# Kernel tuning notes

Hardware: AMD Instinct MI355X
Metric: run time of the kernel (lower is better)

The kernel has to match this reference:

```python
import jax, jax.numpy as jnp
import numpy as np

# Multi-scale feature pyramid spatial shapes (h, w) per level; static for jit.
SPATIAL_SHAPES = np.array([[64, 176], [32, 88], [16, 44], [8, 22]], dtype=np.int32)


def setup_inputs() -> dict:
    key = jax.random.key(0)
    k1, k2 = jax.random.split(key)
    bs, num_heads, head_dim = 6, 8, 32          # 6 cams, embed_dim 256
    num_queries, num_levels, num_points = 40000, 4, 4  # 200x200 BEV grid, 4 Z anchors
    num_keys = int((SPATIAL_SHAPES[:, 0] * SPATIAL_SHAPES[:, 1]).sum())  # 14960
    value = jax.random.normal(k1, (bs, num_keys, num_heads, head_dim), jnp.float32)
    # normalized sampling locations in [0,1] (x, y)
    sampling_locations = jax.random.uniform(
        k2, (bs, num_queries, num_heads, num_levels, num_points, 2), jnp.float32)
    value_spatial_shapes = jnp.asarray(SPATIAL_SHAPES)
    return {"value": value,
            "value_spatial_shapes": value_spatial_shapes,
            "sampling_locations": sampling_locations}


def _msda(value, sampling_locations):
    """Multi-scale deformable attention, nearest sampling, zero padding,
    align_corners=False (matches F.grid_sample defaults used in the source).
    value: (bs, num_keys, H, D); sampling_locations: (bs, nq, H, L, P, 2).
    Returns (bs, nq, H*D)."""
    bs, _, H, D = value.shape
    _, nq, _, num_levels, P, _ = sampling_locations.shape
    grids = 2.0 * sampling_locations - 1.0  # -> [-1, 1]
    out = jnp.zeros((bs, H, nq, D), value.dtype)
    offset = 0
    for lvl in range(num_levels):
        h, w = int(SPATIAL_SHAPES[lvl, 0]), int(SPATIAL_SHAPES[lvl, 1])
        # (bs, h*w, H, D) -> (bs, H, h*w, D)
        v = jnp.transpose(value[:, offset:offset + h * w], (0, 2, 1, 3))
        g = grids[:, :, :, lvl]                      # (bs, nq, H, P, 2)
        # unnormalize (align_corners=False): pix = ((g+1)*size - 1)/2
        x = (g[..., 0] + 1.0) * w * 0.5 - 0.5
        y = (g[..., 1] + 1.0) * h * 0.5 - 0.5
        ix = jnp.rint(x).astype(jnp.int32)
        iy = jnp.rint(y).astype(jnp.int32)
        valid = (ix >= 0) & (ix < w) & (iy >= 0) & (iy < h)
        idx = jnp.clip(iy, 0, h - 1) * w + jnp.clip(ix, 0, w - 1)  # (bs, nq, H, P)
        idx = jnp.transpose(idx, (0, 2, 1, 3)).reshape(bs, H, nq * P)
        sampled = jnp.take_along_axis(v, idx[..., None], axis=2)  # (bs, H, nq*P, D)
        mask = jnp.transpose(valid, (0, 2, 1, 3)).reshape(bs, H, nq * P, 1)
        sampled = jnp.where(mask, sampled, 0.0).reshape(bs, H, nq, P, D)
        out = out + sampled.sum(axis=3)  # sum over points; accumulating over levels
        offset += h * w
    # (bs, H, nq, D) -> (bs, nq, H*D)
    return jnp.transpose(out, (0, 2, 1, 3)).reshape(bs, nq, H * D)


def reference(value, value_spatial_shapes, sampling_locations):
    # value_spatial_shapes matches the static SPATIAL_SHAPES constant used for
    # level splitting (shapes must be static under jit).
    return _msda(value, sampling_locations)
```

## Files before the change

### kernel.cpp

```cpp
#include <hip/hip_runtime.h>


#define BS 6
#define NQ 40000
#define NH 8
#define HD 32
#define NK 14960

typedef float f32x4 __attribute__((ext_vector_type(4)));

__global__ __launch_bounds__(256, 4)
void msda_kernel(const float* __restrict__ value,
                 const float* __restrict__ loc,
                 float* __restrict__ out) {
    const int tid = blockIdx.x * 256 + threadIdx.x;
    const int dg  = tid & 7;
    const int g   = tid >> 3;
    const int h   = g & 7;
    const int bq  = g >> 3;
    const int b   = bq / NQ;

    const int lane = threadIdx.x & 63;
    const int ll   = lane & 7;

    const f32x4 myL = *(const f32x4*)(loc + (size_t)g * 32 + ll * 4);

    const int l   = ll >> 1;
    const int W   = 176 >> l;
    const int Hh  = 64  >> l;
    const int off = (45056 - (45056 >> (2 * l))) / 3;
    const float wf = (float)W, hf = (float)Hh;

    int koff[2];
    #pragma unroll
    for (int j = 0; j < 2; ++j) {
        const float px = j ? myL.z : myL.x;
        const float py = j ? myL.w : myL.y;
        const float gx = 2.0f * px - 1.0f;
        const float gy = 2.0f * py - 1.0f;
        const float x  = ((gx + 1.0f) * wf) * 0.5f - 0.5f;
        const float y  = ((gy + 1.0f) * hf) * 0.5f - 0.5f;
        const float fx = rintf(x);
        const float fy = rintf(y);
        const int ix = (int)fx;
        const int iy = (int)fy;
        const bool valid = (ix >= 0) & (ix < W) & (iy >= 0) & (iy < Hh);
        const int cx = min(max(ix, 0), W - 1);
        const int cy = min(max(iy, 0), Hh - 1);
        const int key = off + cy * W + cx;
        koff[j] = (key << 10) | (valid ? 1 : 0);
    }

    const int srcbase = lane & 56;
    int ko[16];
    #pragma unroll
    for (int s = 0; s < 16; ++s)
        ko[s] = __shfl(koff[s & 1], srcbase + (s >> 1), 64);

    const unsigned base_off = (unsigned)b * (NK * NH * HD * 4u)
                            + (unsigned)h * (HD * 4u)
                            + (unsigned)dg * 16u;

    f32x4 v[16];
    #pragma unroll
    for (int s = 0; s < 16; ++s) {
        const unsigned a = base_off + ((unsigned)ko[s] & 0xFFFFFFFEu);
        v[s] = *(const f32x4*)((const char*)value + a);
    }
    asm volatile(""
        : "+v"(v[0]),  "+v"(v[1]),  "+v"(v[2]),  "+v"(v[3]),
          "+v"(v[4]),  "+v"(v[5]),  "+v"(v[6]),  "+v"(v[7]),
          "+v"(v[8]),  "+v"(v[9]),  "+v"(v[10]), "+v"(v[11]),
          "+v"(v[12]), "+v"(v[13]), "+v"(v[14]), "+v"(v[15]));

    f32x4 acc = {0.f, 0.f, 0.f, 0.f};
    #pragma unroll
    for (int s = 0; s < 16; ++s) {
        const float w = (float)(ko[s] & 1);
        acc.x = fmaf(v[s].x, w, acc.x);
        acc.y = fmaf(v[s].y, w, acc.y);
        acc.z = fmaf(v[s].z, w, acc.z);
        acc.w = fmaf(v[s].w, w, acc.w);
    }

    *(f32x4*)(out + (size_t)g * HD + dg * 4) = acc;
}

extern "C" void kernel_launch(void* const* d_in, const int* in_sizes, int n_in,
                              void* d_out, int out_size, void* d_ws, size_t ws_size,
                              hipStream_t stream) {
    const float* value = (const float*)d_in[0];
    const float* loc   = (const float*)d_in[2];
    float* out = (float*)d_out;

    msda_kernel<<<60000, 256, 0, stream>>>(value, loc, out);
}
```

Baseline: 620.6 us.

## Process two query-head groups per thread with nontemporal loc loads and output stores

Each thread now handles two (batch,query,head) groups 32 apart, issuing 32 gathered value loads in flight instead of 16. The grid is halved and the launch bound is relaxed to allow more registers. Validity bits are packed into a bitmask, and the streaming location reads and output writes use nontemporal hints to keep value data resident in cache. This buys more memory-level parallelism per thread at the cost of higher register pressure and lower occupancy.

```diff
diff --git a/kernel.cpp b/kernel.cpp
--- a/kernel.cpp
+++ b/kernel.cpp
@@ -9,21 +9,24 @@
 
 typedef float f32x4 __attribute__((ext_vector_type(4)));
 
-__global__ __launch_bounds__(256, 4)
+__global__ __launch_bounds__(256, 2)
 void msda_kernel(const float* __restrict__ value,
                  const float* __restrict__ loc,
                  float* __restrict__ out) {
-    const int tid = blockIdx.x * 256 + threadIdx.x;
-    const int dg  = tid & 7;
-    const int g   = tid >> 3;
-    const int h   = g & 7;
-    const int bq  = g >> 3;
-    const int b   = bq / NQ;
+    const int t  = threadIdx.x;
+    const int ll = t & 7;
+    const int gi = t >> 3;
+    const int g0 = blockIdx.x * 64 + gi;
+    const int g1 = g0 + 32;
+    const int h  = g0 & 7;
+    const int b  = g0 / 320000;
 
-    const int lane = threadIdx.x & 63;
-    const int ll   = lane & 7;
+    const int lane = t & 63;
 
-    const f32x4 myL = *(const f32x4*)(loc + (size_t)g * 32 + ll * 4);
+    const f32x4 L0 = __builtin_nontemporal_load(
+        (const f32x4*)(loc + (size_t)g0 * 32 + ll * 4));
+    const f32x4 L1 = __builtin_nontemporal_load(
+        (const f32x4*)(loc + (size_t)g1 * 32 + ll * 4));
 
     const int l   = ll >> 1;
     const int W   = 176 >> l;
@@ -31,59 +34,91 @@
     const int off = (45056 - (45056 >> (2 * l))) / 3;
     const float wf = (float)W, hf = (float)Hh;
 
-    int koff[2];
+    int k0[2], k1[2];
     #pragma unroll
-    for (int j = 0; j < 2; ++j) {
-        const float px = j ? myL.z : myL.x;
-        const float py = j ? myL.w : myL.y;
-        const float gx = 2.0f * px - 1.0f;
-        const float gy = 2.0f * py - 1.0f;
-        const float x  = ((gx + 1.0f) * wf) * 0.5f - 0.5f;
-        const float y  = ((gy + 1.0f) * hf) * 0.5f - 0.5f;
-        const float fx = rintf(x);
-        const float fy = rintf(y);
-        const int ix = (int)fx;
-        const int iy = (int)fy;
-        const bool valid = (ix >= 0) & (ix < W) & (iy >= 0) & (iy < Hh);
-        const int cx = min(max(ix, 0), W - 1);
-        const int cy = min(max(iy, 0), Hh - 1);
-        const int key = off + cy * W + cx;
-        koff[j] = (key << 10) | (valid ? 1 : 0);
+    for (int grp = 0; grp < 2; ++grp) {
+        const f32x4 Lv = grp ? L1 : L0;
+        #pragma unroll
+        for (int j = 0; j < 2; ++j) {
+            const float px = j ? Lv.z : Lv.x;
+            const float py = j ? Lv.w : Lv.y;
+            const float gx = 2.0f * px - 1.0f;
+            const float gy = 2.0f * py - 1.0f;
+            const float x  = ((gx + 1.0f) * wf) * 0.5f - 0.5f;
+            const float y  = ((gy + 1.0f) * hf) * 0.5f - 0.5f;
+            const float fx = rintf(x);
+            const float fy = rintf(y);
+            const int ix = (int)fx;
+            const int iy = (int)fy;
+            const bool valid = (ix >= 0) & (ix < W) & (iy >= 0) & (iy < Hh);
+            const int cx = min(max(ix, 0), W - 1);
+            const int cy = min(max(iy, 0), Hh - 1);
+            const int key = off + cy * W + cx;
+            const int packed = (key << 10) | (valid ? 1 : 0);
+            (grp ? k1 : k0)[j] = packed;
+        }
     }
 
     const int srcbase = lane & 56;
-    int ko[16];
+    int ko0[16], ko1[16];
+    int wm0 = 0, wm1 = 0;
     #pragma unroll
-    for (int s = 0; s < 16; ++s)
-        ko[s] = __shfl(koff[s & 1], srcbase + (s >> 1), 64);
+    for (int s = 0; s < 16; ++s) {
+        const int a0 = __shfl(k0[s & 1], srcbase + (s >> 1), 64);
+        const int a1 = __shfl(k1[s & 1], srcbase + (s >> 1), 64);
+        ko0[s] = a0 & ~1;
+        ko1[s] = a1 & ~1;
+        wm0 |= (a0 & 1) << s;
+        wm1 |= (a1 & 1) << s;
+    }
 
     const unsigned base_off = (unsigned)b * (NK * NH * HD * 4u)
                             + (unsigned)h * (HD * 4u)
-                            + (unsigned)dg * 16u;
+                            + (unsigned)ll * 16u;
+    const char* vb = (const char*)value;
 
-    f32x4 v[16];
+    f32x4 v0[16], v1[16];
+    #pragma unroll
+    for (int s = 0; s < 16; ++s)
+        v0[s] = *(const f32x4*)(vb + (base_off + (unsigned)ko0[s]));
+    #pragma unroll
+    for (int s = 0; s < 16; ++s)
+        v1[s] = *(const f32x4*)(vb + (base_off + (unsigned)ko1[s]));
+
+    asm volatile(""
+        : "+v"(v1[0]),  "+v"(v1[1]),  "+v"(v1[2]),  "+v"(v1[3]),
+          "+v"(v1[4]),  "+v"(v1[5]),  "+v"(v1[6]),  "+v"(v1[7]),
+          "+v"(v1[8]),  "+v"(v1[9]),  "+v"(v1[10]), "+v"(v1[11]),
+          "+v"(v1[12]), "+v"(v1[13]), "+v"(v1[14]), "+v"(v1[15])
+        :
+        : "memory");
+    asm volatile(""
+        : "+v"(v0[0]),  "+v"(v0[1]),  "+v"(v0[2]),  "+v"(v0[3]),
+          "+v"(v0[4]),  "+v"(v0[5]),  "+v"(v0[6]),  "+v"(v0[7]),
+          "+v"(v0[8]),  "+v"(v0[9]),  "+v"(v0[10]), "+v"(v0[11]),
+          "+v"(v0[12]), "+v"(v0[13]), "+v"(v0[14]), "+v"(v0[15]));
+
+    f32x4 acc0 = {0.f, 0.f, 0.f, 0.f};
     #pragma unroll
     for (int s = 0; s < 16; ++s) {
-        const unsigned a = base_off + ((unsigned)ko[s] & 0xFFFFFFFEu);
-        v[s] = *(const f32x4*)((const char*)value + a);
+        const float w = (float)((wm0 >> s) & 1);
+        acc0.x = fmaf(v0[s].x, w, acc0.x);
+        acc0.y = fmaf(v0[s].y, w, acc0.y);
+        acc0.z = fmaf(v0[s].z, w, acc0.z);
+        acc0.w = fmaf(v0[s].w, w, acc0.w);
     }
-    asm volatile(""
-        : "+v"(v[0]),  "+v"(v[1]),  "+v"(v[2]),  "+v"(v[3]),
-          "+v"(v[4]),  "+v"(v[5]),  "+v"(v[6]),  "+v"(v[7]),
-          "+v"(v[8]),  "+v"(v[9]),  "+v"(v[10]), "+v"(v[11]),
-          "+v"(v[12]), "+v"(v[13]), "+v"(v[14]), "+v"(v[15]));
-
-    f32x4 acc = {0.f, 0.f, 0.f, 0.f};
+    f32x4 acc1 = {0.f, 0.f, 0.f, 0.f};
     #pragma unroll
     for (int s = 0; s < 16; ++s) {
-        const float w = (float)(ko[s] & 1);
-        acc.x = fmaf(v[s].x, w, acc.x);
-        acc.y = fmaf(v[s].y, w, acc.y);
-        acc.z = fmaf(v[s].z, w, acc.z);
-        acc.w = fmaf(v[s].w, w, acc.w);
+        const float w = (float)((wm1 >> s) & 1);
+        acc1.x = fmaf(v1[s].x, w, acc1.x);
+        acc1.y = fmaf(v1[s].y, w, acc1.y);
+        acc1.z = fmaf(v1[s].z, w, acc1.z);
+        acc1.w = fmaf(v1[s].w, w, acc1.w);
     }
 
-    *(f32x4*)(out + (size_t)g * HD + dg * 4) = acc;
+    __builtin_nontemporal_store(acc0, (f32x4*)(out + (size_t)g0 * HD + ll * 4));
+    __builtin_nontemporal_store(acc1, (f32x4*)(out + (size_t)g1 * HD + ll * 4));
 }
 
 extern "C" void kernel_launch(void* const* d_in, const int* in_sizes, int n_in,
@@ -93,5 +128,5 @@
     const float* loc   = (const float*)d_in[2];
     float* out = (float*)d_out;
 
-    msda_kernel<<<60000, 256, 0, stream>>>(value, loc, out);
+    msda_kernel<<<30000, 256, 0, stream>>>(value, loc, out);
 }
```

Measured after the change: 609.1 us. No clear change (-1.8%).
